# Kernel tuning notes

Hardware: AMD Instinct MI355X
Metric: run time of the kernel (lower is better)

Reference implementation:

```python
import jax, jax.numpy as jnp
import numpy as np

B, T, D, H, W = 2, 8192, 512, 8, 256
d = D // H  # 64
NC = T // W  # number of chunks (T divisible by W)


def setup_inputs() -> dict:
    key = jax.random.key(0)
    ks = jax.random.split(key, 9)
    s = 1.0 / np.sqrt(D).astype(np.float32)
    x = jax.random.normal(ks[0], (B, T, D), jnp.float32)
    Wq = jax.random.normal(ks[1], (D, D), jnp.float32) * s
    Wk = jax.random.normal(ks[2], (D, D), jnp.float32) * s
    Wv = jax.random.normal(ks[3], (D, D), jnp.float32) * s
    Wo = jax.random.normal(ks[4], (D, D), jnp.float32) * s
    bq = jax.random.normal(ks[5], (D,), jnp.float32) * 0.01
    bk = jax.random.normal(ks[6], (D,), jnp.float32) * 0.01
    bv = jax.random.normal(ks[7], (D,), jnp.float32) * 0.01
    bo = jax.random.normal(ks[8], (D,), jnp.float32) * 0.01
    return {"x": x, "Wq": Wq, "bq": bq, "Wk": Wk, "bk": bk,
            "Wv": Wv, "bv": bv, "Wo": Wo, "bo": bo}


def _local_attention(q, k, v):
    # q, k, v: [B, H, T, d]. Each W-sized query chunk attends to keys in
    # [chunk_start - W, chunk_end + W) -> a 3W window, masked at boundaries.
    qc = q.reshape(B, H, NC, W, d)
    pad = ((0, 0), (0, 0), (W, W), (0, 0))
    kp = jnp.pad(k, pad)
    vp = jnp.pad(v, pad)
    # window gather indices into padded sequence: [NC, 3W]
    pos = jnp.arange(NC)[:, None] * W + jnp.arange(3 * W)[None, :]
    kw = kp[:, :, pos, :]  # [B, H, NC, 3W, d]
    vw = vp[:, :, pos, :]  # [B, H, NC, 3W, d]
    valid = (pos >= W) & (pos < T + W)  # [NC, 3W] true for real (unpadded) keys
    scores = jnp.einsum('bhcqd,bhckd->bhcqk', qc, kw) * (d ** -0.5)
    scores = jnp.where(valid[None, None, :, None, :], scores, -jnp.inf)
    attn = jax.nn.softmax(scores, axis=-1)
    out = jnp.einsum('bhcqk,bhckd->bhcqd', attn, vw)
    return out.reshape(B, H, T, d)


def reference(x, Wq, bq, Wk, bk, Wv, bv, Wo, bo):
    # Linear = x @ W.T + b (torch nn.Linear convention)
    q = (x @ Wq.T + bq).reshape(B, T, H, d).transpose(0, 2, 1, 3)
    # k_proj / v_proj run under torch.no_grad() in the original
    k = jax.lax.stop_gradient(x @ Wk.T + bk).reshape(B, T, H, d).transpose(0, 2, 1, 3)
    v = jax.lax.stop_gradient(x @ Wv.T + bv).reshape(B, T, H, d).transpose(0, 2, 1, 3)
    out = _local_attention(q, k, v)           # [B, H, T, d]
    out = out.transpose(0, 2, 1, 3).reshape(B, T, D)
    return out @ Wo.T + bo
```

## Files before the change

### kernel.cpp

```cpp
#include <hip/hip_runtime.h>
#include <hip/hip_bf16.h>

typedef unsigned short u16;
typedef unsigned int   u32;
typedef __bf16 bf16x8 __attribute__((ext_vector_type(8)));
typedef float  f32x4  __attribute__((ext_vector_type(4)));

#define BB 2
#define TT 8192
#define DD 512
#define HH 8
#define WW 256
#define DH 64
#define NX 8388608
#define NW 262144

__device__ __forceinline__ float b2f(u16 u) {
    unsigned int x = ((unsigned int)u) << 16;
    return __builtin_bit_cast(float, x);
}
__device__ __forceinline__ u16 f2b(float f) {
    __bf16 h = (__bf16)f;
    return __builtin_bit_cast(u16, h);
}
__device__ __forceinline__ bf16x8 ldsfrag(const u16* p) {
    return *(const bf16x8*)p;
}
__device__ __forceinline__ f32x4 mfma16(bf16x8 a, bf16x8 b, f32x4 c) {
    return __builtin_amdgcn_mfma_f32_16x16x32_bf16(a, b, c, 0, 0, 0);
}

typedef __attribute__((address_space(1))) u32 gu32;
typedef __attribute__((address_space(3))) u32 lu32;
__device__ __forceinline__ void gl_lds(const u16* g, u16* l) {
#if defined(__has_builtin) && __has_builtin(__builtin_amdgcn_global_load_lds)
    __builtin_amdgcn_global_load_lds((gu32*)g, (lu32*)l, 16, 0, 0);
#else
    const int lane = threadIdx.x & 63;
    *(uint4*)(l + lane * 8) = *(const uint4*)g;
#endif
}

__global__ void detect_dtype(const u16* __restrict__ x, int* __restrict__ flag)
{
    __shared__ int bad;
    if (threadIdx.x == 0) bad = 0;
    __syncthreads();
    int mybad = 0;
    for (int i = threadIdx.x; i < 4096; i += 256) {
        float v = b2f(x[i]);
        if (!(fabsf(v) < 100.f)) mybad = 1;
    }
    if (mybad) atomicOr(&bad, 1);
    __syncthreads();
    if (threadIdx.x == 0) *flag = bad ? 1 : 0;
}

__device__ __forceinline__ u16 cvt1(const void* s, long i, int f) {
    return f ? f2b(((const float*)s)[i]) : ((const u16*)s)[i];
}

__global__ void convert_all(const void* x, const void* Wq, const void* bq,
                            const void* Wk, const void* bk, const void* Wv,
                            const void* bv, const void* Wo, const void* bo,
                            u16* __restrict__ xb, u16* __restrict__ Wcat,
                            u16* __restrict__ Wob, u16* __restrict__ bcat,
                            u16* __restrict__ bob, const int* __restrict__ flagp)
{
    const int f = *flagp;
    long i = (long)blockIdx.x * 256 + threadIdx.x;
    if (i < NX) { xb[i] = cvt1(x, i, f); return; }
    i -= NX;
    if (i < NW) { Wcat[i] = cvt1(Wq, i, f); return; }
    i -= NW;
    if (i < NW) { Wcat[NW + i] = cvt1(Wk, i, f); return; }
    i -= NW;
    if (i < NW) { Wcat[2 * NW + i] = cvt1(Wv, i, f); return; }
    i -= NW;
    if (i < NW) { Wob[i] = cvt1(Wo, i, f); return; }
    i -= NW;
    if (i < 512)  { bcat[i] = cvt1(bq, i, f); return; }
    i -= 512;
    if (i < 512)  { bcat[512 + i] = cvt1(bk, i, f); return; }
    i -= 512;
    if (i < 512)  { bcat[1024 + i] = cvt1(bv, i, f); return; }
    i -= 512;
    if (i < 512)  { bob[i] = cvt1(bo, i, f); }
}

__global__ __launch_bounds__(256, 2)
void gemm128(const u16* __restrict__ A, const u16* __restrict__ Bw,
             const u16* __restrict__ bias, void* __restrict__ out0,
             u16* __restrict__ out1, u16* __restrict__ out2,
             int mode, const int* __restrict__ flagp)
{
    __shared__ __align__(16) u16 AsF[128 * 64];
    __shared__ __align__(16) u16 BsF[128 * 64];

    const int tid  = threadIdx.x;
    const int lane = tid & 63;
    const int wv   = tid >> 6;
    const int col  = lane & 15;
    const int quad = lane >> 4;
    const int wm   = (wv & 1) * 64;
    const int wn   = (wv >> 1) * 64;
    const int m0   = blockIdx.x * 128;
    const int n0   = blockIdx.y * 128;

    f32x4 acc[4][4] = {};

    for (int k0 = 0; k0 < 512; k0 += 64) {
        __syncthreads();
        #pragma unroll
        for (int i = 0; i < 4; i++) {
            const int r  = (wv * 4 + i) * 8 + (lane >> 3);
            const int cb = (lane & 7) ^ (r & 7);
            gl_lds(A  + (size_t)(m0 + r) * 512 + k0 + cb * 8, &AsF[(wv * 4 + i) * 512]);
            gl_lds(Bw + (size_t)(n0 + r) * 512 + k0 + cb * 8, &BsF[(wv * 4 + i) * 512]);
        }
        __syncthreads();
        #pragma unroll
        for (int kk = 0; kk < 2; kk++) {
            bf16x8 fa[4], fb[4];
            #pragma unroll
            for (int mi = 0; mi < 4; mi++)
                fa[mi] = ldsfrag(&AsF[(wm + mi * 16 + col) * 64 + ((kk * 4 + quad) ^ (col & 7)) * 8]);
            #pragma unroll
            for (int ni = 0; ni < 4; ni++)
                fb[ni] = ldsfrag(&BsF[(wn + ni * 16 + col) * 64 + ((kk * 4 + quad) ^ (col & 7)) * 8]);
            #pragma unroll
            for (int mi = 0; mi < 4; mi++)
                #pragma unroll
                for (int ni = 0; ni < 4; ni++)
                    acc[mi][ni] = mfma16(fa[mi], fb[ni], acc[mi][ni]);
        }
    }

    if (mode == 0) {
        #pragma unroll
        for (int ni = 0; ni < 4; ni++) {
            const int gn = n0 + wn + ni * 16 + col;
            const float bv = b2f(bias[gn]);
            const int seg = gn >> 9;
            #pragma unroll
            for (int mi = 0; mi < 4; mi++) {
                const int gmb = m0 + wm + mi * 16 + quad * 4;
                if (seg < 2) {
                    u16* dst = (seg == 0) ? (u16*)out0 : out1;
                    #pragma unroll
                    for (int r = 0; r < 4; r++)
                        dst[(size_t)(gmb + r) * 512 + (gn & 511)] = f2b(acc[mi][ni][r] + bv);
                } else {
                    const int d = gn & 63, hh = (gn >> 6) & 7;
                    const int bb = gmb >> 13, t = gmb & 8191;
                    u16 pb[4];
                    #pragma unroll
                    for (int r = 0; r < 4; r++) pb[r] = f2b(acc[mi][ni][r] + bv);
                    uint2 pk;
                    pk.x = pb[0] | ((u32)pb[1] << 16);
                    pk.y = pb[2] | ((u32)pb[3] << 16);
                    *(uint2*)&out2[((size_t)(bb * 8 + hh) * 64 + d) * 8192 + t] = pk;
                }
            }
        }
    } else {
        const int outf32 = *flagp;
        #pragma unroll
        for (int ni = 0; ni < 4; ni++) {
            const int gn = n0 + wn + ni * 16 + col;
            const float bv = b2f(bias[gn]);
            #pragma unroll
            for (int mi = 0; mi < 4; mi++) {
                #pragma unroll
                for (int r = 0; r < 4; r++) {
                    const int gm = m0 + wm + mi * 16 + quad * 4 + r;
                    const float v = acc[mi][ni][r] + bv;
                    if (outf32) ((float*)out0)[(size_t)gm * 512 + gn] = v;
                    else        ((u16*)out0)[(size_t)gm * 512 + gn]  = f2b(v);
                }
            }
        }
    }
}

#define PSW 72
__global__ __launch_bounds__(256, 2)
void attn_local(const u16* __restrict__ Qg, const u16* __restrict__ Kg,
                const u16* __restrict__ VTg, u16* __restrict__ Og)
{
    __shared__ __align__(16) u16 Ks[64 * 64];
    __shared__ __align__(16) u16 VTs[64 * 64];
    __shared__ __align__(16) u16 Ps[4 * 64 * PSW];

    const int tid  = threadIdx.x;
    const int lane = tid & 63;
    const int wv   = tid >> 6;
    const int col  = lane & 15;
    const int quad = lane >> 4;

    const int idx = blockIdx.x;
    const int c = idx & 31;
    const int h = (idx >> 5) & 7;
    const int b = idx >> 8;

    const int t0 = c * WW;
    const int wq = wv * 64;

    bf16x8 qf[4][2];
    {
        const size_t qbase = ((size_t)(b * TT + t0 + wq + col)) * DD + h * DH + quad * 8;
        #pragma unroll
        for (int qi = 0; qi < 4; qi++)
            #pragma unroll
            for (int kk = 0; kk < 2; kk++)
                qf[qi][kk] = *(const bf16x8*)(Qg + qbase + (size_t)qi * 16 * DD + kk * 32);
    }

    f32x4 o[4][4] = {};
    float lsum[4] = {0.f, 0.f, 0.f, 0.f};

    u16* psb = &Ps[wv * 64 * PSW];

    for (int sc = 0; sc < 12; sc++) {
        const int kstart = t0 - WW + sc * 64;
        if (kstart < 0 || kstart >= TT) continue;
        __syncthreads();
        #pragma unroll
        for (int i = 0; i < 2; i++) {
            const int r  = (wv * 2 + i) * 8 + (lane >> 3);
            const int cb = (lane & 7) ^ (r & 7);
            gl_lds(Kg  + ((size_t)(b * TT + kstart + r)) * DD + h * DH + cb * 8,
                   &Ks[(wv * 2 + i) * 512]);
            gl_lds(VTg + ((size_t)((b * HH + h) * DH + r)) * TT + kstart + cb * 8,
                   &VTs[(wv * 2 + i) * 512]);
        }
        __syncthreads();

        f32x4 s[4][4];
        #pragma unroll
        for (int ns = 0; ns < 4; ns++)
            #pragma unroll
            for (int qi = 0; qi < 4; qi++)
                s[ns][qi] = (f32x4){0.f, 0.f, 0.f, 0.f};
        #pragma unroll
        for (int ns = 0; ns < 4; ns++) {
            const int row = ns * 16 + col;
            bf16x8 ka0 = ldsfrag(&Ks[row * 64 + ((0 + quad) ^ (col & 7)) * 8]);
            bf16x8 ka1 = ldsfrag(&Ks[row * 64 + ((4 + quad) ^ (col & 7)) * 8]);
            #pragma unroll
            for (int qi = 0; qi < 4; qi++) {
                s[ns][qi] = mfma16(ka0, qf[qi][0], s[ns][qi]);
                s[ns][qi] = mfma16(ka1, qf[qi][1], s[ns][qi]);
            }
        }

        #pragma unroll
        for (int ns = 0; ns < 4; ns++) {
            #pragma unroll
            for (int qi = 0; qi < 4; qi++) {
                u16 pb[4];
                #pragma unroll
                for (int r = 0; r < 4; r++) {
                    const float p = __expf(s[ns][qi][r] * 0.125f);
                    pb[r] = f2b(p);
                    lsum[qi] += b2f(pb[r]);
                }
                uint2 pk;
                pk.x = pb[0] | ((u32)pb[1] << 16);
                pk.y = pb[2] | ((u32)pb[3] << 16);
                *(uint2*)&psb[(qi * 16 + col) * PSW + ns * 16 + quad * 4] = pk;
            }
        }
        asm volatile("" ::: "memory");

        #pragma unroll
        for (int kt = 0; kt < 2; kt++) {
            bf16x8 pf[4];
            #pragma unroll
            for (int qi = 0; qi < 4; qi++)
                pf[qi] = ldsfrag(&psb[(qi * 16 + col) * PSW + kt * 32 + quad * 8]);
            #pragma unroll
            for (int di = 0; di < 4; di++) {
                bf16x8 va = ldsfrag(&VTs[(di * 16 + col) * 64 + ((kt * 4 + quad) ^ (col & 7)) * 8]);
                #pragma unroll
                for (int qi = 0; qi < 4; qi++)
                    o[di][qi] = mfma16(va, pf[qi], o[di][qi]);
            }
        }
    }

    #pragma unroll
    for (int qi = 0; qi < 4; qi++) {
        float l = lsum[qi];
        l += __shfl_xor(l, 16);
        l += __shfl_xor(l, 32);
        lsum[qi] = 1.0f / l;
    }

    #pragma unroll
    for (int qi = 0; qi < 4; qi++) {
        const size_t ob = ((size_t)(b * TT + t0 + wq + qi * 16 + col)) * DD + h * DH + quad * 4;
        #pragma unroll
        for (int di = 0; di < 4; di++) {
            u16 pb[4];
            #pragma unroll
            for (int r = 0; r < 4; r++) pb[r] = f2b(o[di][qi][r] * lsum[qi]);
            uint2 pk;
            pk.x = pb[0] | ((u32)pb[1] << 16);
            pk.y = pb[2] | ((u32)pb[3] << 16);
            *(uint2*)&Og[ob + di * 16] = pk;
        }
    }
}

extern "C" void kernel_launch(void* const* d_in, const int* in_sizes, int n_in,
                              void* d_out, int out_size, void* d_ws, size_t ws_size,
                              hipStream_t stream)
{
    u16* ws   = (u16*)d_ws;
    u16* xb   = ws;
    u16* Wcat = xb + NX;
    u16* Wob  = Wcat + 3 * NW;
    u16* bcat = Wob + NW;
    u16* bob  = bcat + 1536;
    u16* qws  = bob + 512;
    u16* kws  = qws + NX;
    u16* vtws = kws + NX;
    u16* aws  = vtws + NX;
    int* flag = (int*)(aws + NX);

    detect_dtype<<<1, 256, 0, stream>>>((const u16*)d_in[0], flag);

    convert_all<<<36872, 256, 0, stream>>>(
        d_in[0], d_in[1], d_in[2], d_in[3], d_in[4], d_in[5], d_in[6], d_in[7], d_in[8],
        xb, Wcat, Wob, bcat, bob, flag);

    gemm128<<<dim3(128, 12), 256, 0, stream>>>(xb, Wcat, bcat, qws, kws, vtws, 0, flag);
    attn_local<<<dim3(BB * HH * 32), 256, 0, stream>>>(qws, kws, vtws, aws);
    gemm128<<<dim3(128, 4), 256, 0, stream>>>(aws, Wob, bob, d_out, nullptr, nullptr, 1, flag);
}
```

Measured before the change: 208.5 us.

## Double-buffer attention K/V tiles, vectorize conversion and fold dtype detection into it

The local-attention kernel now double-buffers its K and V^T LDS tiles. It issues the async global-to-LDS load for the next 64-key tile before computing on the current one, which drops one barrier per iteration and removes the per-iteration boundary checks. The input conversion kernel now handles 8 elements per thread with 16-byte loads and stores, and the separate dtype-detection launch is folded into it. In exchange, every block re-reads a small prefix of x to decide the dtype, and LDS use per block grows. The softmax denominator now sums fp32 probabilities instead of bf16-rounded ones, a small numeric change.

Measured after the change: 196.8 us. 5.6% less time.

```diff
diff --git a/kernel.cpp b/kernel.cpp
--- a/kernel.cpp
+++ b/kernel.cpp
@@ -33,31 +33,27 @@
 typedef __attribute__((address_space(1))) u32 gu32;
 typedef __attribute__((address_space(3))) u32 lu32;
 __device__ __forceinline__ void gl_lds(const u16* g, u16* l) {
-#if defined(__has_builtin) && __has_builtin(__builtin_amdgcn_global_load_lds)
     __builtin_amdgcn_global_load_lds((gu32*)g, (lu32*)l, 16, 0, 0);
-#else
-    const int lane = threadIdx.x & 63;
-    *(uint4*)(l + lane * 8) = *(const uint4*)g;
-#endif
-}
-
-__global__ void detect_dtype(const u16* __restrict__ x, int* __restrict__ flag)
-{
-    __shared__ int bad;
-    if (threadIdx.x == 0) bad = 0;
-    __syncthreads();
-    int mybad = 0;
-    for (int i = threadIdx.x; i < 4096; i += 256) {
-        float v = b2f(x[i]);
-        if (!(fabsf(v) < 100.f)) mybad = 1;
-    }
-    if (mybad) atomicOr(&bad, 1);
-    __syncthreads();
-    if (threadIdx.x == 0) *flag = bad ? 1 : 0;
-}
-
-__device__ __forceinline__ u16 cvt1(const void* s, long i, int f) {
-    return f ? f2b(((const float*)s)[i]) : ((const u16*)s)[i];
+}
+
+__device__ __forceinline__ void cvt8(const void* s, u16* d, long i, int f) {
+    if (f) {
+        const u32* sp = (const u32*)s + i;
+        uint4 a = *(const uint4*)(sp);
+        uint4 b = *(const uint4*)(sp + 4);
+        u16 o[8];
+        o[0] = f2b(__builtin_bit_cast(float, a.x));
+        o[1] = f2b(__builtin_bit_cast(float, a.y));
+        o[2] = f2b(__builtin_bit_cast(float, a.z));
+        o[3] = f2b(__builtin_bit_cast(float, a.w));
+        o[4] = f2b(__builtin_bit_cast(float, b.x));
+        o[5] = f2b(__builtin_bit_cast(float, b.y));
+        o[6] = f2b(__builtin_bit_cast(float, b.z));
+        o[7] = f2b(__builtin_bit_cast(float, b.w));
+        *(uint4*)(d + i) = *(const uint4*)o;
+    } else {
+        *(uint4*)(d + i) = *(const uint4*)((const u16*)s + i);
+    }
 }
 
 __global__ void convert_all(const void* x, const void* Wq, const void* bq,
@@ -65,27 +61,40 @@
                             const void* bv, const void* Wo, const void* bo,
                             u16* __restrict__ xb, u16* __restrict__ Wcat,
                             u16* __restrict__ Wob, u16* __restrict__ bcat,
-                            u16* __restrict__ bob, const int* __restrict__ flagp)
+                            u16* __restrict__ bob, int* __restrict__ flagw)
 {
-    const int f = *flagp;
-    long i = (long)blockIdx.x * 256 + threadIdx.x;
-    if (i < NX) { xb[i] = cvt1(x, i, f); return; }
+    __shared__ int sflag;
+    const int tid = threadIdx.x;
+    if (tid == 0) sflag = 0;
+    __syncthreads();
+    int mybad = 0;
+    for (int i = tid; i < 2048; i += 256) {
+        float v = b2f(((const u16*)x)[i]);
+        if (!(fabsf(v) < 100.f)) mybad = 1;
+    }
+    if (mybad) atomicOr(&sflag, 1);
+    __syncthreads();
+    const int f = sflag ? 1 : 0;
+    if (blockIdx.x == 0 && tid == 0) *flagw = f;
+
+    long i = ((long)blockIdx.x * 256 + tid) * 8;
+    if (i < NX)            { cvt8(x,  xb,           i, f); return; }
     i -= NX;
-    if (i < NW) { Wcat[i] = cvt1(Wq, i, f); return; }
+    if (i < NW)            { cvt8(Wq, Wcat,         i, f); return; }
     i -= NW;
-    if (i < NW) { Wcat[NW + i] = cvt1(Wk, i, f); return; }
+    if (i < NW)            { cvt8(Wk, Wcat + NW,    i, f); return; }
     i -= NW;
-    if (i < NW) { Wcat[2 * NW + i] = cvt1(Wv, i, f); return; }
+    if (i < NW)            { cvt8(Wv, Wcat + 2*NW,  i, f); return; }
     i -= NW;
-    if (i < NW) { Wob[i] = cvt1(Wo, i, f); return; }
+    if (i < NW)            { cvt8(Wo, Wob,          i, f); return; }
     i -= NW;
-    if (i < 512)  { bcat[i] = cvt1(bq, i, f); return; }
+    if (i < 512)           { cvt8(bq, bcat,         i, f); return; }
     i -= 512;
-    if (i < 512)  { bcat[512 + i] = cvt1(bk, i, f); return; }
+    if (i < 512)           { cvt8(bk, bcat + 512,   i, f); return; }
     i -= 512;
-    if (i < 512)  { bcat[1024 + i] = cvt1(bv, i, f); return; }
+    if (i < 512)           { cvt8(bv, bcat + 1024,  i, f); return; }
     i -= 512;
-    if (i < 512)  { bob[i] = cvt1(bo, i, f); }
+    if (i < 512)           { cvt8(bo, bob,          i, f); }
 }
 
 __global__ __launch_bounds__(256, 2)
@@ -188,9 +197,9 @@
 void attn_local(const u16* __restrict__ Qg, const u16* __restrict__ Kg,
                 const u16* __restrict__ VTg, u16* __restrict__ Og)
 {
-    __shared__ __align__(16) u16 Ks[64 * 64];
-    __shared__ __align__(16) u16 VTs[64 * 64];
-    __shared__ __align__(16) u16 Ps[4 * 64 * PSW];
+    __shared__ __align__(16) u16 Ks[2][64 * 64];
+    __shared__ __align__(16) u16 VTs[2][64 * 64];
+    __shared__ __align__(16) u16 Ps[4][64 * PSW];
 
     const int tid  = threadIdx.x;
     const int lane = tid & 63;
@@ -206,6 +215,12 @@
     const int t0 = c * WW;
     const int wq = wv * 64;
 
+    const int sc_lo = (c == 0) ? 4 : 0;
+    const int nsc   = (c == 0 || c == 31) ? 8 : 12;
+
+    const int ldr = lane >> 3;
+    const int ldc = lane & 7;
+
     bf16x8 qf[4][2];
     {
         const size_t qbase = ((size_t)(b * TT + t0 + wq + col)) * DD + h * DH + quad * 8;
@@ -219,22 +234,38 @@
     f32x4 o[4][4] = {};
     float lsum[4] = {0.f, 0.f, 0.f, 0.f};
 
-    u16* psb = &Ps[wv * 64 * PSW];
-
-    for (int sc = 0; sc < 12; sc++) {
-        const int kstart = t0 - WW + sc * 64;
-        if (kstart < 0 || kstart >= TT) continue;
+    u16* psb = &Ps[wv][0];
+
+    {
+        const int kstart = t0 - WW + sc_lo * 64;
+        #pragma unroll
+        for (int i = 0; i < 2; i++) {
+            const int rr = (wv * 2 + i) * 8 + ldr;
+            const int cb = ldc ^ (rr & 7);
+            gl_lds(Kg  + ((size_t)(b * TT + kstart + rr)) * DD + h * DH + cb * 8,
+                   &Ks[0][(wv * 2 + i) * 512]);
+            gl_lds(VTg + ((size_t)((b * HH + h) * DH + rr)) * TT + kstart + cb * 8,
+                   &VTs[0][(wv * 2 + i) * 512]);
+        }
+    }
+
+    for (int it = 0; it < nsc; it++) {
         __syncthreads();
-        #pragma unroll
-        for (int i = 0; i < 2; i++) {
-            const int r  = (wv * 2 + i) * 8 + (lane >> 3);
-            const int cb = (lane & 7) ^ (r & 7);
-            gl_lds(Kg  + ((size_t)(b * TT + kstart + r)) * DD + h * DH + cb * 8,
-                   &Ks[(wv * 2 + i) * 512]);
-            gl_lds(VTg + ((size_t)((b * HH + h) * DH + r)) * TT + kstart + cb * 8,
-                   &VTs[(wv * 2 + i) * 512]);
-        }
-        __syncthreads();
+        if (it + 1 < nsc) {
+            const int kstart = t0 - WW + (sc_lo + it + 1) * 64;
+            const int buf = (it + 1) & 1;
+            #pragma unroll
+            for (int i = 0; i < 2; i++) {
+                const int rr = (wv * 2 + i) * 8 + ldr;
+                const int cb = ldc ^ (rr & 7);
+                gl_lds(Kg  + ((size_t)(b * TT + kstart + rr)) * DD + h * DH + cb * 8,
+                       &Ks[buf][(wv * 2 + i) * 512]);
+                gl_lds(VTg + ((size_t)((b * HH + h) * DH + rr)) * TT + kstart + cb * 8,
+                       &VTs[buf][(wv * 2 + i) * 512]);
+            }
+        }
+        const u16* ks = &Ks[it & 1][0];
+        const u16* vs = &VTs[it & 1][0];
 
         f32x4 s[4][4];
         #pragma unroll
@@ -245,8 +276,8 @@
         #pragma unroll
         for (int ns = 0; ns < 4; ns++) {
             const int row = ns * 16 + col;
-            bf16x8 ka0 = ldsfrag(&Ks[row * 64 + ((0 + quad) ^ (col & 7)) * 8]);
-            bf16x8 ka1 = ldsfrag(&Ks[row * 64 + ((4 + quad) ^ (col & 7)) * 8]);
+            bf16x8 ka0 = ldsfrag(&ks[row * 64 + ((0 + quad) ^ (col & 7)) * 8]);
+            bf16x8 ka1 = ldsfrag(&ks[row * 64 + ((4 + quad) ^ (col & 7)) * 8]);
             #pragma unroll
             for (int qi = 0; qi < 4; qi++) {
                 s[ns][qi] = mfma16(ka0, qf[qi][0], s[ns][qi]);
@@ -263,7 +294,7 @@
                 for (int r = 0; r < 4; r++) {
                     const float p = __expf(s[ns][qi][r] * 0.125f);
                     pb[r] = f2b(p);
-                    lsum[qi] += b2f(pb[r]);
+                    lsum[qi] += p;
                 }
                 uint2 pk;
                 pk.x = pb[0] | ((u32)pb[1] << 16);
@@ -281,7 +312,7 @@
                 pf[qi] = ldsfrag(&psb[(qi * 16 + col) * PSW + kt * 32 + quad * 8]);
             #pragma unroll
             for (int di = 0; di < 4; di++) {
-                bf16x8 va = ldsfrag(&VTs[(di * 16 + col) * 64 + ((kt * 4 + quad) ^ (col & 7)) * 8]);
+                bf16x8 va = ldsfrag(&vs[(di * 16 + col) * 64 + ((kt * 4 + quad) ^ (col & 7)) * 8]);
                 #pragma unroll
                 for (int qi = 0; qi < 4; qi++)
                     o[di][qi] = mfma16(va, pf[qi], o[di][qi]);
@@ -329,9 +360,7 @@
     u16* aws  = vtws + NX;
     int* flag = (int*)(aws + NX);
 
-    detect_dtype<<<1, 256, 0, stream>>>((const u16*)d_in[0], flag);
-
-    convert_all<<<36872, 256, 0, stream>>>(
+    convert_all<<<4609, 256, 0, stream>>>(
         d_in[0], d_in[1], d_in[2], d_in[3], d_in[4], d_in[5], d_in[6], d_in[7], d_in[8],
         xb, Wcat, Wob, bcat, bob, flag);
 
```
